# Performance work log

Hardware: AMD Instinct MI355X
Metric: run time of the kernel (lower is better)

The kernel has to match this reference:

```python
import jax, jax.numpy as jnp
import numpy as np

N_NODES = 100000
N_EDGES = 1600000
IN_DIM = 128
HID = 128
N_CLASSES = 16
N_GRAPHS = 512


def setup_inputs() -> dict:
    key = jax.random.key(0)
    ks = jax.random.split(key, 16)
    d = {
        "x": jax.random.normal(ks[0], (N_NODES, IN_DIM), jnp.float32),
        "src": jax.random.randint(ks[1], (N_EDGES,), 0, N_NODES, jnp.int64 if jax.config.jax_enable_x64 else jnp.int32),
        "dst": jax.random.randint(ks[2], (N_EDGES,), 0, N_NODES, jnp.int64 if jax.config.jax_enable_x64 else jnp.int32),
        "gid": jnp.sort(jax.random.randint(ks[3], (N_NODES,), 0, N_GRAPHS, jnp.int64 if jax.config.jax_enable_x64 else jnp.int32)),
    }
    s = 1.0 / np.sqrt(HID)
    for i, k in zip(range(1, 5), ks[4:8]):
        d[f"W{i}"] = jax.random.uniform(k, (HID, HID), jnp.float32, -s, s)
        d[f"b{i}"] = jnp.zeros((HID,), jnp.float32)
    d["Wv"] = jax.random.uniform(ks[8], (HID, 1), jnp.float32, -s, s)
    d["bv"] = jnp.zeros((1,), jnp.float32)
    d["Wc"] = jax.random.uniform(ks[9], (HID, N_CLASSES), jnp.float32, -s, s)
    d["bc"] = jnp.zeros((N_CLASSES,), jnp.float32)
    return d


def _gcn_layer(h, W, b, src, dst, norm_src, norm_dst):
    # DGL GraphConv, norm='both': D_dst^{-1/2} * A * D_src^{-1/2} * h * W + b, then ReLU outside
    m = (h * norm_src[:, None])[src]                                  # [E, H] edge gather
    agg = jax.ops.segment_sum(m, dst, num_segments=N_NODES)           # [N, H] scatter-add
    return jax.nn.relu(agg * norm_dst[:, None] @ W + b)


def reference(x, W1, b1, W2, b2, W3, b3, W4, b4, Wv, bv, Wc, bc, src, dst, gid):
    ones = jnp.ones((N_EDGES,), jnp.float32)
    deg_out = jnp.clip(jax.ops.segment_sum(ones, src, num_segments=N_NODES), 1.0)
    deg_in = jnp.clip(jax.ops.segment_sum(ones, dst, num_segments=N_NODES), 1.0)
    norm_src = jax.lax.rsqrt(deg_out)
    norm_dst = jax.lax.rsqrt(deg_in)

    h = _gcn_layer(x, W1, b1, src, dst, norm_src, norm_dst)
    h = _gcn_layer(h, W2, b2, src, dst, norm_src, norm_dst)
    h = _gcn_layer(h, W3, b3, src, dst, norm_src, norm_dst)
    h = _gcn_layer(h, W4, b4, src, dst, norm_src, norm_dst)

    w = jax.nn.sigmoid(h @ Wv + bv)                                   # [N, 1]
    num = jax.ops.segment_sum(h * w, gid, num_segments=N_GRAPHS)      # [G, H]
    den = jax.ops.segment_sum(w, gid, num_segments=N_GRAPHS)          # [G, 1]
    hg = jnp.where(den > 0, num / jnp.where(den > 0, den, 1.0), 0.0)  # weighted mean readout
    return hg @ Wc + bc                                               # [G, n_classes]
```

## Files before the change

### kernel.cpp

```cpp
#include <hip/hip_runtime.h>
#include <hip/hip_bf16.h>

#define N_NODES_C 100000
#define N_EDGES_C 1600000
#define HID_C 128
#define NCLS_C 16
#define NGRAPH_C 512
#define SCAN_BLK 1024
#define NCHUNK ((N_NODES_C + SCAN_BLK - 1) / SCAN_BLK)
#define FILL_PASSES 4
#define FILL_RANGE ((N_NODES_C + FILL_PASSES - 1) / FILL_PASSES)

__global__ void k_count(const int* __restrict__ src, const int* __restrict__ dst,
                        int* cnt_out, int* cnt_in) {
  int i = blockIdx.x * blockDim.x + threadIdx.x;
  int stride = gridDim.x * blockDim.x;
  for (; i < N_EDGES_C; i += stride) {
    atomicAdd(&cnt_out[src[i]], 1);
    atomicAdd(&cnt_in[dst[i]], 1);
  }
}

__global__ void k_norm(const int* __restrict__ cnt_out, const int* __restrict__ cnt_in,
                       float* norm_src, float* norm_dst) {
  int i = blockIdx.x * blockDim.x + threadIdx.x;
  if (i < N_NODES_C) {
    norm_src[i] = 1.f / sqrtf(fmaxf((float)cnt_out[i], 1.f));
    norm_dst[i] = 1.f / sqrtf(fmaxf((float)cnt_in[i], 1.f));
  }
}

__global__ void k_scan1(const int* __restrict__ cnt, int* part) {
  __shared__ int s[SCAN_BLK];
  int tid = threadIdx.x;
  int i = blockIdx.x * SCAN_BLK + tid;
  s[tid] = (i < N_NODES_C) ? cnt[i] : 0;
  __syncthreads();
  for (int off = SCAN_BLK / 2; off > 0; off >>= 1) {
    if (tid < off) s[tid] += s[tid + off];
    __syncthreads();
  }
  if (tid == 0) part[blockIdx.x] = s[0];
}

__global__ void k_scan2(int* part, int* row_start) {
  if (threadIdx.x == 0 && blockIdx.x == 0) {
    int run = 0;
    for (int i = 0; i < NCHUNK; ++i) { int v = part[i]; part[i] = run; run += v; }
    row_start[N_NODES_C] = run;
  }
}

__global__ void k_scan3(const int* __restrict__ cnt, const int* __restrict__ part,
                        int* row_start, int* cursor) {
  __shared__ int s[SCAN_BLK];
  int tid = threadIdx.x;
  int i = blockIdx.x * SCAN_BLK + tid;
  int x = (i < N_NODES_C) ? cnt[i] : 0;
  s[tid] = x;
  __syncthreads();
  for (int off = 1; off < SCAN_BLK; off <<= 1) {
    int v = (tid >= off) ? s[tid - off] : 0;
    __syncthreads();
    s[tid] += v;
    __syncthreads();
  }
  if (i < N_NODES_C) {
    int excl = part[blockIdx.x] + s[tid] - x;
    row_start[i] = excl;
    cursor[i] = excl;
  }
}

__global__ void k_fill(const int* __restrict__ src, const int* __restrict__ dst,
                       int* cursor, int* __restrict__ csr_src) {
  int tid0 = blockIdx.x * blockDim.x + threadIdx.x;
  int stride = gridDim.x * blockDim.x;
#pragma unroll 1
  for (int pass = 0; pass < FILL_PASSES; ++pass) {
    int lo = pass * FILL_RANGE;
    int hi = lo + FILL_RANGE;
    for (int i = tid0; i < N_EDGES_C; i += stride) {
      int d = dst[i];
      if (d >= lo && d < hi) {
        int p = atomicAdd(&cursor[d], 1);
        csr_src[p] = src[i];
      }
    }
  }
}

__global__ void k_gstart(const int* __restrict__ gid, int* __restrict__ gstart) {
  int n = blockIdx.x * blockDim.x + threadIdx.x;
  if (n >= N_NODES_C) return;
  int g = gid[n];
  int gp = (n == 0) ? -1 : gid[n - 1];
  for (int k = gp + 1; k <= g; ++k) gstart[k] = n;
  if (n == N_NODES_C - 1) {
    for (int k = g + 1; k <= NGRAPH_C; ++k) gstart[k] = N_NODES_C;
  }
}

__global__ __launch_bounds__(256) void k_gemm_rowscale(
    const float* __restrict__ A, const float* __restrict__ W,
    const float* __restrict__ rowscale, float* __restrict__ T, int rows) {
  __shared__ float sA[32][132];
  __shared__ float sB[32][132];
  int t = threadIdx.x;
  int tx = t & 15, ty = t >> 4;
  int m0 = blockIdx.x * 128;

  float acc[8][8];
#pragma unroll
  for (int i = 0; i < 8; ++i)
#pragma unroll
    for (int j = 0; j < 8; ++j) acc[i][j] = 0.f;

  int ar = t >> 3;
  int ac = (t & 7) * 4;
  int wk = t >> 5;
  int wn = (t & 31) * 4;

  for (int k0 = 0; k0 < HID_C; k0 += 32) {
#pragma unroll
    for (int rr = 0; rr < 4; ++rr) {
      int r = rr * 32 + ar;
      int row = m0 + r;
      float4 v = make_float4(0.f, 0.f, 0.f, 0.f);
      if (row < rows) v = *(const float4*)&A[(size_t)row * HID_C + k0 + ac];
      sA[ac + 0][r] = v.x;
      sA[ac + 1][r] = v.y;
      sA[ac + 2][r] = v.z;
      sA[ac + 3][r] = v.w;
    }
#pragma unroll
    for (int i = 0; i < 4; ++i) {
      int kc = i * 8 + wk;
      float4 v = *(const float4*)&W[(size_t)(k0 + kc) * HID_C + wn];
      *(float4*)&sB[kc][wn] = v;
    }
    __syncthreads();

#pragma unroll 8
    for (int kk = 0; kk < 32; ++kk) {
      float a[8], b[8];
#pragma unroll
      for (int i = 0; i < 8; ++i) a[i] = sA[kk][ty * 8 + i];
#pragma unroll
      for (int j = 0; j < 8; ++j) b[j] = sB[kk][tx * 8 + j];
#pragma unroll
      for (int i = 0; i < 8; ++i)
#pragma unroll
        for (int j = 0; j < 8; ++j) acc[i][j] = fmaf(a[i], b[j], acc[i][j]);
    }
    __syncthreads();
  }

#pragma unroll
  for (int i = 0; i < 8; ++i) {
    int row = m0 + ty * 8 + i;
    if (row < rows) {
      float sc = rowscale[row];
      float4 v0 = {acc[i][0] * sc, acc[i][1] * sc, acc[i][2] * sc, acc[i][3] * sc};
      float4 v1 = {acc[i][4] * sc, acc[i][5] * sc, acc[i][6] * sc, acc[i][7] * sc};
      float4* p = (float4*)&T[(size_t)row * HID_C + tx * 8];
      p[0] = v0;
      p[1] = v1;
    }
  }
}

__global__ __launch_bounds__(256) void k_agg(
    const float* __restrict__ T, const int* __restrict__ row_start,
    const int* __restrict__ csr_src, const float* __restrict__ norm_dst,
    const float* __restrict__ bias, float* __restrict__ H) {
  int wid = threadIdx.x >> 6, lane = threadIdx.x & 63;
  int n = blockIdx.x * 4 + wid;
  if (n >= N_NODES_C) return;
  int s0 = row_start[n], s1 = row_start[n + 1];
  const float2* T2 = (const float2*)T;
  float ax = 0.f, ay = 0.f;
  int e = s0;
  for (; e + 8 <= s1; e += 8) {
    int a0 = csr_src[e + 0], a1 = csr_src[e + 1];
    int a2 = csr_src[e + 2], a3 = csr_src[e + 3];
    int a4 = csr_src[e + 4], a5 = csr_src[e + 5];
    int a6 = csr_src[e + 6], a7 = csr_src[e + 7];
    float2 v0 = T2[(size_t)a0 * 64 + lane];
    float2 v1 = T2[(size_t)a1 * 64 + lane];
    float2 v2 = T2[(size_t)a2 * 64 + lane];
    float2 v3 = T2[(size_t)a3 * 64 + lane];
    float2 v4 = T2[(size_t)a4 * 64 + lane];
    float2 v5 = T2[(size_t)a5 * 64 + lane];
    float2 v6 = T2[(size_t)a6 * 64 + lane];
    float2 v7 = T2[(size_t)a7 * 64 + lane];
    ax += v0.x + v1.x + v2.x + v3.x + v4.x + v5.x + v6.x + v7.x;
    ay += v0.y + v1.y + v2.y + v3.y + v4.y + v5.y + v6.y + v7.y;
  }
  for (; e < s1; ++e) {
    int a = csr_src[e];
    float2 v = T2[(size_t)a * 64 + lane];
    ax += v.x;
    ay += v.y;
  }
  float nd = norm_dst[n];
  float bx = bias[2 * lane], by = bias[2 * lane + 1];
  float2 r;
  r.x = fmaxf(fmaf(ax, nd, bx), 0.f);
  r.y = fmaxf(fmaf(ay, nd, by), 0.f);
  ((float2*)H)[(size_t)n * 64 + lane] = r;
}

__global__ __launch_bounds__(256) void k_readout(
    const float* __restrict__ H, const float* __restrict__ Wv,
    const float* __restrict__ bv, const int* __restrict__ gstart,
    const float* __restrict__ Wc, const float* __restrict__ bc,
    float* __restrict__ out) {
  int g = blockIdx.x;
  int wid = threadIdx.x >> 6, lane = threadIdx.x & 63;
  int s0 = gstart[g], s1 = gstart[g + 1];
  float2 wv2 = ((const float2*)Wv)[lane];
  float bvs = bv[0];
  float ax = 0.f, ay = 0.f, dw = 0.f;
  for (int n = s0 + wid; n < s1; n += 4) {
    float2 h2 = ((const float2*)H)[(size_t)n * 64 + lane];
    float p = h2.x * wv2.x + h2.y * wv2.y;
#pragma unroll
    for (int off = 32; off > 0; off >>= 1) p += __shfl_xor(p, off);
    float w = 1.f / (1.f + expf(-(p + bvs)));
    ax += h2.x * w;
    ay += h2.y * w;
    dw += w;
  }
  __shared__ float2 snum[4][64];
  __shared__ float sden[4];
  __shared__ float hg[HID_C];
  snum[wid][lane] = make_float2(ax, ay);
  if (lane == 0) sden[wid] = dw;
  __syncthreads();
  if (wid == 0) {
    float2 a = snum[0][lane], b = snum[1][lane], c = snum[2][lane], d = snum[3][lane];
    float den = sden[0] + sden[1] + sden[2] + sden[3];
    float inv = (den > 0.f) ? 1.f / den : 0.f;
    hg[2 * lane] = (a.x + b.x + c.x + d.x) * inv;
    hg[2 * lane + 1] = (a.y + b.y + c.y + d.y) * inv;
  }
  __syncthreads();
  if (threadIdx.x < NCLS_C) {
    int c = threadIdx.x;
    float acc = 0.f;
    for (int k = 0; k < HID_C; ++k) acc = fmaf(hg[k], Wc[k * NCLS_C + c], acc);
    out[g * NCLS_C + c] = acc + bc[c];
  }
}

extern "C" void kernel_launch(void* const* d_in, const int* in_sizes, int n_in,
                              void* d_out, int out_size, void* d_ws, size_t ws_size,
                              hipStream_t stream) {
  const float* x = (const float*)d_in[0];
  const int* src = (const int*)d_in[1];
  const int* dst = (const int*)d_in[2];
  const int* gid = (const int*)d_in[3];
  const float* W[4] = {(const float*)d_in[4], (const float*)d_in[6],
                       (const float*)d_in[8], (const float*)d_in[10]};
  const float* b[4] = {(const float*)d_in[5], (const float*)d_in[7],
                       (const float*)d_in[9], (const float*)d_in[11]};
  const float* Wv = (const float*)d_in[12];
  const float* bv = (const float*)d_in[13];
  const float* Wc = (const float*)d_in[14];
  const float* bc = (const float*)d_in[15];
  float* out = (float*)d_out;

  char* ws = (char*)d_ws;
  size_t off = 0;
  auto alloc = [&](size_t bytes) -> char* {
    char* p = ws + off;
    off = (off + bytes + 255) & ~(size_t)255;
    return p;
  };
  int* cnt_out = (int*)alloc((size_t)N_NODES_C * 4);
  int* cnt_in = (int*)alloc((size_t)N_NODES_C * 4);
  float* norm_src = (float*)alloc((size_t)N_NODES_C * 4);
  float* norm_dst = (float*)alloc((size_t)N_NODES_C * 4);
  int* row_start = (int*)alloc((size_t)(N_NODES_C + 1) * 4);
  int* cursor = (int*)alloc((size_t)N_NODES_C * 4);
  int* part = (int*)alloc((size_t)SCAN_BLK * 4);
  int* gstart = (int*)alloc((size_t)(NGRAPH_C + 1) * 4);
  int* csr_src = (int*)alloc((size_t)N_EDGES_C * 4);
  float* tbuf = (float*)alloc((size_t)N_NODES_C * HID_C * 4);
  float* hbuf = (float*)alloc((size_t)N_NODES_C * HID_C * 4);
  (void)ws_size;
  (void)in_sizes;
  (void)n_in;
  (void)out_size;

  hipMemsetAsync(cnt_out, 0, (size_t)N_NODES_C * 4, stream);
  hipMemsetAsync(cnt_in, 0, (size_t)N_NODES_C * 4, stream);

  k_count<<<2048, 256, 0, stream>>>(src, dst, cnt_out, cnt_in);
  k_norm<<<(N_NODES_C + 255) / 256, 256, 0, stream>>>(cnt_out, cnt_in, norm_src, norm_dst);
  k_scan1<<<NCHUNK, SCAN_BLK, 0, stream>>>(cnt_in, part);
  k_scan2<<<1, 1, 0, stream>>>(part, row_start);
  k_scan3<<<NCHUNK, SCAN_BLK, 0, stream>>>(cnt_in, part, row_start, cursor);
  k_fill<<<2048, 256, 0, stream>>>(src, dst, cursor, csr_src);
  k_gstart<<<(N_NODES_C + 255) / 256, 256, 0, stream>>>(gid, gstart);

  int gemm_grid = (N_NODES_C + 127) / 128;
  int node_grid = (N_NODES_C + 3) / 4;
  const float* hin = x;
  for (int l = 0; l < 4; ++l) {
    k_gemm_rowscale<<<gemm_grid, 256, 0, stream>>>(hin, W[l], norm_src, tbuf, N_NODES_C);
    k_agg<<<node_grid, 256, 0, stream>>>(tbuf, row_start, csr_src, norm_dst, b[l], hbuf);
    hin = hbuf;
  }

  k_readout<<<NGRAPH_C, 256, 0, stream>>>(hbuf, Wv, bv, gstart, Wc, bc, out);
}
```

Measured before the change: 922.5 us.

## Widen GEMM K-tile with vectorized swizzled LDS reads and split degree counting

The row-scaled GEMM now stages a K-tile of 64 instead of 32 and reads A and W from shared memory as float4 vectors. The W tile uses a column swizzle to avoid bank conflicts, which halves the number of barriers and the count of LDS instructions in the inner loop. Degree counting is split into separate src and dst kernels that load indices as int4, with one thread per four edges. The cost is more shared memory per block, which may lower occupancy, and an extra kernel launch.

```diff
diff --git a/kernel.cpp b/kernel.cpp
--- a/kernel.cpp
+++ b/kernel.cpp
@@ -11,13 +11,25 @@
 #define FILL_PASSES 4
 #define FILL_RANGE ((N_NODES_C + FILL_PASSES - 1) / FILL_PASSES)
 
-__global__ void k_count(const int* __restrict__ src, const int* __restrict__ dst,
-                        int* cnt_out, int* cnt_in) {
+__global__ void k_count_src(const int* __restrict__ src, int* cnt_out) {
   int i = blockIdx.x * blockDim.x + threadIdx.x;
-  int stride = gridDim.x * blockDim.x;
-  for (; i < N_EDGES_C; i += stride) {
-    atomicAdd(&cnt_out[src[i]], 1);
-    atomicAdd(&cnt_in[dst[i]], 1);
+  if (i < N_EDGES_C / 4) {
+    int4 v = ((const int4*)src)[i];
+    atomicAdd(&cnt_out[v.x], 1);
+    atomicAdd(&cnt_out[v.y], 1);
+    atomicAdd(&cnt_out[v.z], 1);
+    atomicAdd(&cnt_out[v.w], 1);
+  }
+}
+
+__global__ void k_count_dst(const int* __restrict__ dst, int* cnt_in) {
+  int i = blockIdx.x * blockDim.x + threadIdx.x;
+  if (i < N_EDGES_C / 4) {
+    int4 v = ((const int4*)dst)[i];
+    atomicAdd(&cnt_in[v.x], 1);
+    atomicAdd(&cnt_in[v.y], 1);
+    atomicAdd(&cnt_in[v.z], 1);
+    atomicAdd(&cnt_in[v.w], 1);
   }
 }
 
@@ -101,11 +113,15 @@
   }
 }
 
+__device__ __forceinline__ int swz_col(int n) {
+  return (n < 64) ? n : 64 + ((n - 60) & 63);
+}
+
 __global__ __launch_bounds__(256) void k_gemm_rowscale(
     const float* __restrict__ A, const float* __restrict__ W,
     const float* __restrict__ rowscale, float* __restrict__ T, int rows) {
-  __shared__ float sA[32][132];
-  __shared__ float sB[32][132];
+  __shared__ float sA[64][132];
+  __shared__ float sB[64][128];
   int t = threadIdx.x;
   int tx = t & 15, ty = t >> 4;
   int m0 = blockIdx.x * 128;
@@ -116,38 +132,43 @@
 #pragma unroll
     for (int j = 0; j < 8; ++j) acc[i][j] = 0.f;
 
-  int ar = t >> 3;
-  int ac = (t & 7) * 4;
-  int wk = t >> 5;
-  int wn = (t & 31) * 4;
-
-  for (int k0 = 0; k0 < HID_C; k0 += 32) {
-#pragma unroll
-    for (int rr = 0; rr < 4; ++rr) {
-      int r = rr * 32 + ar;
+  int a_c4 = (t & 15) * 4;
+  int a_r = t >> 4;
+  int w_n4 = (t & 31) * 4;
+  int w_k = t >> 5;
+  int w_ns = swz_col(w_n4);
+
+  int b0 = swz_col(tx * 8);
+  int b1 = swz_col(tx * 8 + 4);
+
+  for (int k0 = 0; k0 < HID_C; k0 += 64) {
+#pragma unroll
+    for (int rr = 0; rr < 8; ++rr) {
+      int r = rr * 16 + a_r;
       int row = m0 + r;
       float4 v = make_float4(0.f, 0.f, 0.f, 0.f);
-      if (row < rows) v = *(const float4*)&A[(size_t)row * HID_C + k0 + ac];
-      sA[ac + 0][r] = v.x;
-      sA[ac + 1][r] = v.y;
-      sA[ac + 2][r] = v.z;
-      sA[ac + 3][r] = v.w;
-    }
-#pragma unroll
-    for (int i = 0; i < 4; ++i) {
-      int kc = i * 8 + wk;
-      float4 v = *(const float4*)&W[(size_t)(k0 + kc) * HID_C + wn];
-      *(float4*)&sB[kc][wn] = v;
-    }
-    __syncthreads();
-
-#pragma unroll 8
-    for (int kk = 0; kk < 32; ++kk) {
-      float a[8], b[8];
-#pragma unroll
-      for (int i = 0; i < 8; ++i) a[i] = sA[kk][ty * 8 + i];
-#pragma unroll
-      for (int j = 0; j < 8; ++j) b[j] = sB[kk][tx * 8 + j];
+      if (row < rows) v = *(const float4*)&A[(size_t)row * HID_C + k0 + a_c4];
+      sA[a_c4 + 0][r] = v.x;
+      sA[a_c4 + 1][r] = v.y;
+      sA[a_c4 + 2][r] = v.z;
+      sA[a_c4 + 3][r] = v.w;
+    }
+#pragma unroll
+    for (int i = 0; i < 8; ++i) {
+      int kc = i * 8 + w_k;
+      float4 v = *(const float4*)&W[(size_t)(k0 + kc) * HID_C + w_n4];
+      *(float4*)&sB[kc][w_ns] = v;
+    }
+    __syncthreads();
+
+#pragma unroll 2
+    for (int kk = 0; kk < 64; ++kk) {
+      float4 a0 = *(const float4*)&sA[kk][ty * 8];
+      float4 a1 = *(const float4*)&sA[kk][ty * 8 + 4];
+      float4 bb0 = *(const float4*)&sB[kk][b0];
+      float4 bb1 = *(const float4*)&sB[kk][b1];
+      float a[8] = {a0.x, a0.y, a0.z, a0.w, a1.x, a1.y, a1.z, a1.w};
+      float b[8] = {bb0.x, bb0.y, bb0.z, bb0.w, bb1.x, bb1.y, bb1.z, bb1.w};
 #pragma unroll
       for (int i = 0; i < 8; ++i)
 #pragma unroll
@@ -297,7 +318,9 @@
   hipMemsetAsync(cnt_out, 0, (size_t)N_NODES_C * 4, stream);
   hipMemsetAsync(cnt_in, 0, (size_t)N_NODES_C * 4, stream);
 
-  k_count<<<2048, 256, 0, stream>>>(src, dst, cnt_out, cnt_in);
+  int count_grid = (N_EDGES_C / 4 + 255) / 256;
+  k_count_src<<<count_grid, 256, 0, stream>>>(src, cnt_out);
+  k_count_dst<<<count_grid, 256, 0, stream>>>(dst, cnt_in);
   k_norm<<<(N_NODES_C + 255) / 256, 256, 0, stream>>>(cnt_out, cnt_in, norm_src, norm_dst);
   k_scan1<<<NCHUNK, SCAN_BLK, 0, stream>>>(cnt_in, part);
   k_scan2<<<1, 1, 0, stream>>>(part, row_start);
```

Result: slower. 968.8 us (+5.0%).
